# Kernel tuning notes

Hardware: AMD Instinct MI355X
Metric: run time of the kernel (lower is better)

Reference implementation:

```python
import jax, jax.numpy as jnp
import numpy as np
from jax import lax

# Per-tensor power-of-two scales (ScalingImplType.CONST / POWER_OF_TWO in Brevitas)
S_ACT8 = 2.0 ** -4   # 8-bit signed input quant scale
S_ACT4 = 2.0 ** -1   # 4-bit signed input quant scale
S_W = 2.0 ** -2      # per-tensor weight quant scale
S_RELU = 2.0 ** -2   # 4-bit unsigned QuantReLU scale


def fq(x, scale, qmin, qmax):
    # fake-quant with straight-through estimator (STE)
    q = jnp.clip(jnp.round(x / scale), qmin, qmax) * scale
    return x + lax.stop_gradient(q - x)


def fq_signed(x, scale, bits):
    return fq(x, scale, -(2 ** (bits - 1)), 2 ** (bits - 1) - 1)


def fq_uint(x, scale, bits):
    return fq(x, scale, 0, 2 ** bits - 1)


def qconv(x, w, in_bits, w_bits, s_in, stride=1, padding=0, groups=1):
    xq = fq_signed(x, s_in, in_bits)
    wq = fq_signed(w, S_W, w_bits)
    return lax.conv_general_dilated(
        xq, wq, (stride, stride), [(padding, padding)] * 2,
        feature_group_count=groups,
        dimension_numbers=('NCHW', 'OIHW', 'NCHW'))


def maxpool(x, k, s):
    return lax.reduce_window(x, -jnp.inf, lax.max,
                             (1, 1, k, k), (1, 1, s, s), 'VALID')


def dwsep(x, dw, pw):
    c = x.shape[1]
    x = qconv(x, dw, 4, 4, S_ACT4, padding=1, groups=c)  # depthwise 3x3
    x = qconv(x, pw, 4, 4, S_ACT4)                       # pointwise 1x1
    return x


def qrelu4(x):
    return fq_uint(jax.nn.relu(x), S_RELU, 4)


def setup_inputs() -> dict:
    key = jax.random.key(0)
    ks = jax.random.split(key, 10)
    B = 1024
    mk = lambda k, shp, sc=0.5: jax.random.normal(k, shp, jnp.float32) * sc
    return {
        'x': jax.random.normal(ks[0], (B, 3, 32, 32), jnp.float32),
        'w0': mk(ks[1], (3, 3, 1, 1)),
        'dw1': mk(ks[2], (3, 1, 3, 3)),
        'pw1': mk(ks[3], (32, 3, 1, 1)),
        'dw2': mk(ks[4], (32, 1, 3, 3)),
        'pw2': mk(ks[5], (64, 32, 1, 1)),
        'dw3': mk(ks[6], (64, 1, 3, 3)),
        'pw3': mk(ks[7], (128, 64, 1, 1)),
        'wc1': mk(ks[8], (256, 128, 1, 1)),
        'wc2': mk(ks[9], (10, 256, 1, 1)),
    }


def reference(x, w0, dw1, pw1, dw2, pw2, dw3, pw3, wc1, wc2):
    # features
    h = qconv(x, w0, 8, 8, S_ACT8)            # 1x1, 3->3, 8-bit
    h = dwsep(h, dw1, pw1)                    # 3->32, 32x32
    h = qrelu4(h)
    h = maxpool(h, 2, 2)                      # 16x16
    h = dwsep(h, dw2, pw2)                    # 32->64
    h = qrelu4(h)
    h = maxpool(h, 2, 2)                      # 8x8
    h = dwsep(h, dw3, pw3)                    # 64->128
    h = qrelu4(h)
    h = maxpool(h, 8, 1)                      # 1x1
    # classifier
    h = qconv(h, wc1, 4, 4, S_ACT4)           # 128->256
    h = qrelu4(h)
    h = qconv(h, wc2, 4, 4, S_ACT4)           # 256->10
    h = fq_signed(h, S_ACT8, 8)               # output quant int8
    return h
```

## Files before the change

kernel.cpp:

```cpp
#include <hip/hip_runtime.h>

typedef int v4i __attribute__((ext_vector_type(4)));

#define W0i   0
#define DW1i  9
#define PW1i  36
#define DW2i  132
#define DW3i  420
#define PW2p  996
#define PW3p  1508
#define WC1p  3556
#define WC2p  11748
#define PW2Fb 12388
#define PW3Fb 12900
#define WTOT  14948

__device__ __forceinline__ int iclamp(int v, int lo, int hi) {
  return v < lo ? lo : (v > hi ? hi : v);
}
__device__ __forceinline__ int rne4(int a) {
  return (a + 1 + ((a >> 2) & 1)) >> 2;
}
__device__ __forceinline__ int rne32(int a) {
  return (a + 15 + ((a >> 5) & 1)) >> 5;
}

__device__ __forceinline__ int dot4(int a, int b, int c) {
#if defined(__has_builtin) && __has_builtin(__builtin_amdgcn_sdot4)
  return __builtin_amdgcn_sdot4(a, b, c, false);
#else
  c += ((a << 24) >> 24) * ((b << 24) >> 24);
  c += ((a << 16) >> 24) * ((b << 16) >> 24);
  c += ((a <<  8) >> 24) * ((b <<  8) >> 24);
  c += (a >> 24) * (b >> 24);
  return c;
#endif
}

__device__ __forceinline__ int alignb(int hi, int lo, int sh) {
#if defined(__has_builtin) && __has_builtin(__builtin_amdgcn_alignbyte)
  return __builtin_amdgcn_alignbyte(hi, lo, sh);
#else
  return (int)(((((unsigned long long)(unsigned)hi) << 32) |
                (unsigned)lo) >> (8 * sh));
#endif
}

__device__ __forceinline__ int pack3(int a, int b, int c) {
  return (a & 0xff) | ((b & 0xff) << 8) | ((c & 0xff) << 16);
}

__global__ __launch_bounds__(256) void prep_weights(
    const float* __restrict__ w0,  const float* __restrict__ dw1,
    const float* __restrict__ pw1, const float* __restrict__ dw2,
    const float* __restrict__ pw2, const float* __restrict__ dw3,
    const float* __restrict__ pw3, const float* __restrict__ wc1,
    const float* __restrict__ wc2, int* __restrict__ ws) {
  int t = blockIdx.x * blockDim.x + threadIdx.x;
  if (t >= WTOT) return;
  if (t < PW2p) {
    float w; int lo = -8, hi = 7;
    if (t < DW1i)      { w = w0[t];        lo = -128; hi = 127; }
    else if (t < PW1i)   w = dw1[t - DW1i];
    else if (t < DW2i)   w = pw1[t - PW1i];
    else if (t < DW3i)   w = dw2[t - DW2i];
    else                 w = dw3[t - DW3i];
    ws[t] = iclamp((int)rintf(w * 4.f), lo, hi);
  } else if (t < PW2Fb) {
    const float* src;
    if (t < WC1p) {
      if (t < PW3p) src = pw2 + (t - PW2p) * 4;
      else          src = pw3 + (t - PW3p) * 4;
    } else {
      if (t < WC2p) src = wc1 + (t - WC1p) * 4;
      else          src = wc2 + (t - WC2p) * 4;
    }
    int p = 0;
#pragma unroll
    for (int b = 0; b < 4; b++) {
      int c = iclamp((int)rintf(src[b] * 4.f), -8, 7);
      p |= (c & 0xff) << (8 * b);
    }
    ws[t] = p;
  } else if (t < PW3Fb) {
    int i = t - PW2Fb;
    int nt = i >> 7, r = i & 127, lane = r >> 1, dw = r & 1;
    int n = nt * 16 + (lane & 15);
    int kb = (lane >> 4) * 8 + dw * 4;
    int p = 0;
#pragma unroll
    for (int b = 0; b < 4; b++) {
      int c = iclamp((int)rintf(pw2[n * 32 + kb + b] * 4.f), -8, 7);
      p |= (c & 0xff) << (8 * b);
    }
    ws[t] = p;
  } else {
    int i = t - PW3Fb;
    int g = i >> 7, r = i & 127, lane = r >> 1, dw = r & 1;
    int nt = g >> 1, kh = g & 1;
    int n = nt * 16 + (lane & 15);
    int kb = kh * 32 + (lane >> 4) * 8 + dw * 4;
    int p = 0;
#pragma unroll
    for (int b = 0; b < 4; b++) {
      int c = iclamp((int)rintf(pw3[n * 64 + kb + b] * 4.f), -8, 7);
      p |= (c & 0xff) << (8 * b);
    }
    ws[t] = p;
  }
}

__global__ __launch_bounds__(256, 4) void fused_net(
    const float* __restrict__ x,
    const int*   __restrict__ wq,
    float* __restrict__ out)
{
  const int img = blockIdx.x;
  const int tid = threadIdx.x;

  __shared__ __align__(16) int bufAi[2560];
  __shared__ __align__(16) int bufBi[2592];
  __shared__ int s_red[256];

  {
    const float* xim = x + (size_t)img * 3072;
    const int p4 = tid * 4;
    float4 v0 = *(const float4*)(xim + p4);
    float4 v1 = *(const float4*)(xim + 1024 + p4);
    float4 v2 = *(const float4*)(xim + 2048 + p4);
    int w[9];
#pragma unroll
    for (int i = 0; i < 9; i++) w[i] = wq[W0i + i];
#define Q8(v) iclamp((int)rintf((v) * 16.f), -128, 127)
    int a0[4] = {Q8(v0.x), Q8(v0.y), Q8(v0.z), Q8(v0.w)};
    int a1[4] = {Q8(v1.x), Q8(v1.y), Q8(v1.z), Q8(v1.w)};
    int a2[4] = {Q8(v2.x), Q8(v2.y), Q8(v2.z), Q8(v2.w)};
#undef Q8
#pragma unroll
    for (int o = 0; o < 3; o++) {
      int pk = 0;
#pragma unroll
      for (int j = 0; j < 4; j++) {
        int s = a0[j] * w[o * 3] + a1[j] * w[o * 3 + 1] + a2[j] * w[o * 3 + 2];
        pk |= (iclamp(rne32(s), -8, 7) & 0xff) << (8 * j);
      }
      bufAi[o * 256 + tid] = pk;
    }
  }
  __syncthreads();

  {
    const int y = tid >> 3, q = tid & 7;
#pragma unroll
    for (int c = 0; c < 3; c++) {
      int wr[3];
#pragma unroll
      for (int r = 0; r < 3; r++)
        wr[r] = pack3(wq[DW1i + c * 9 + r * 3], wq[DW1i + c * 9 + r * 3 + 1],
                      wq[DW1i + c * 9 + r * 3 + 2]);
      const int* ap = bufAi + c * 256;
      int acc0 = 0, acc1 = 0, acc2 = 0, acc3 = 0;
#pragma unroll
      for (int ky = 0; ky < 3; ky++) {
        int yy = y + ky - 1;
        if (yy < 0 || yy > 31) continue;
        int base = yy * 8 + q;
        int dC = ap[base];
        int dL = q ? ap[base - 1] : 0;
        int dR = (q < 7) ? ap[base + 1] : 0;
        int w = wr[ky];
        acc0 = dot4(alignb(dC, dL, 3), w, acc0);
        acc1 = dot4(dC, w, acc1);
        acc2 = dot4(alignb(dR, dC, 1), w, acc2);
        acc3 = dot4(alignb(dR, dC, 2), w, acc3);
      }
      int pk = (iclamp(rne4(acc0), -8, 7) & 0xff) |
               ((iclamp(rne4(acc1), -8, 7) & 0xff) << 8) |
               ((iclamp(rne4(acc2), -8, 7) & 0xff) << 16) |
               ((iclamp(rne4(acc3), -8, 7) & 0xff) << 24);
      bufBi[c * 256 + tid] = pk;
    }
  }
  __syncthreads();

  {
    const int py = tid >> 4, px = tid & 15;
    const signed char* bB = (const signed char*)bufBi;
    int a[4];
#pragma unroll
    for (int d = 0; d < 4; d++) {
      int sp = (2 * py + (d >> 1)) * 32 + 2 * px + (d & 1);
      a[d] = pack3(bB[sp], bB[1024 + sp], bB[2048 + sp]);
    }
#pragma unroll
    for (int it = 0; it < 8; it++) {
      int pk = 0;
#pragma unroll
      for (int j = 0; j < 4; j++) {
        int o = it * 4 + j;
        int wpk = pack3(wq[PW1i + o * 3], wq[PW1i + o * 3 + 1],
                        wq[PW1i + o * 3 + 2]);
        int m0 = dot4(a[0], wpk, 0), m1 = dot4(a[1], wpk, 0);
        int m2 = dot4(a[2], wpk, 0), m3 = dot4(a[3], wpk, 0);
        int mx = max(max(m0, m1), max(m2, m3));
        pk |= iclamp(rne4(mx), 0, 7) << (8 * j);
      }
      bufAi[py * 149 + px * 9 + it] = pk;
    }
  }
  __syncthreads();

  for (int it2 = 0; it2 < 2; it2++) {
    int idx = tid + 256 * it2;
    int cq = __builtin_amdgcn_readfirstlane(idx >> 6);
    int s = idx & 63;
    int y = s >> 2, x0 = (s & 3) << 2;
    int wk[9][4];
#pragma unroll
    for (int t9 = 0; t9 < 9; t9++)
#pragma unroll
      for (int cc = 0; cc < 4; cc++)
        wk[t9][cc] = wq[DW2i + (cq * 4 + cc) * 9 + t9];
    int acc[4][4] = {};
#pragma unroll
    for (int ky = 0; ky < 3; ky++) {
      int yy = y + ky - 1;
      if (yy < 0 || yy > 15) continue;
      int rb = yy * 149 + cq;
      int rd[6];
      rd[0] = (x0 > 0) ? bufAi[rb + (x0 - 1) * 9] : 0;
      rd[1] = bufAi[rb + x0 * 9];
      rd[2] = bufAi[rb + (x0 + 1) * 9];
      rd[3] = bufAi[rb + (x0 + 2) * 9];
      rd[4] = bufAi[rb + (x0 + 3) * 9];
      rd[5] = (x0 < 12) ? bufAi[rb + (x0 + 4) * 9] : 0;
      int e[6][4];
#pragma unroll
      for (int k = 0; k < 6; k++)
#pragma unroll
        for (int cc = 0; cc < 4; cc++) e[k][cc] = (rd[k] >> (8 * cc)) & 0xf;
#pragma unroll
      for (int j = 0; j < 4; j++)
#pragma unroll
        for (int kx = 0; kx < 3; kx++)
#pragma unroll
          for (int cc = 0; cc < 4; cc++)
            acc[j][cc] += e[j + kx][cc] * wk[ky * 3 + kx][cc];
    }
#pragma unroll
    for (int j = 0; j < 4; j++) {
      int pk = 0;
#pragma unroll
      for (int cc = 0; cc < 4; cc++)
        pk |= (iclamp(rne4(acc[j][cc]), -8, 7) & 0xff) << (8 * cc);
      bufBi[y * 162 + (x0 + j) * 10 + cq] = pk;
    }
  }
  __syncthreads();

#pragma unroll
  for (int i = 0; i < 4; i++) {
    int id = tid + 256 * i;
    int m = id >> 2, c2 = id & 3;
    int qp = m >> 2, d = m & 3;
    int sy = ((qp >> 3) << 1) + (d >> 1);
    int sx = ((qp & 7) << 1) + (d & 1);
    long v = *(const long*)(bufBi + sy * 162 + sx * 10 + c2 * 2);
    *(long*)(bufAi + m * 10 + c2 * 2) = v;
  }
  __syncthreads();

  {
    const int w = tid >> 6, lane = tid & 63;
    const int lm = lane & 15, kg = lane >> 4;
    const long bw = *(const long*)(wq + PW2Fb + (w * 64 + lane) * 2);
    const signed char* Ab = (const signed char*)bufAi;
    signed char* A2c = (signed char*)bufBi;
    const int n = w * 16 + lm;
#pragma unroll 4
    for (int mt = 0; mt < 16; mt++) {
      int m = mt * 16 + lm;
      long av = *(const long*)(Ab + m * 40 + kg * 8);
      v4i d = __builtin_amdgcn_mfma_i32_16x16x32_i8(av, bw, (v4i){0, 0, 0, 0},
                                                    0, 0, 0);
      int mx = max(max(d[0], d[1]), max(d[2], d[3]));
      int qp = mt * 4 + kg;
      int py = qp >> 3, px = qp & 7;
      A2c[(py * 137 + px * 17 + (n >> 2)) * 4 + (n & 3)] =
          (signed char)iclamp(rne4(mx), 0, 7);
    }
  }
  __syncthreads();

  {
    int cq2 = tid >> 4;
    int s = tid & 15;
    int y = s >> 1, x0 = (s & 1) << 2;
    int wk[9][4];
#pragma unroll
    for (int t9 = 0; t9 < 9; t9++)
#pragma unroll
      for (int cc = 0; cc < 4; cc++)
        wk[t9][cc] = wq[DW3i + (cq2 * 4 + cc) * 9 + t9];
    int acc[4][4] = {};
#pragma unroll
    for (int ky = 0; ky < 3; ky++) {
      int yy = y + ky - 1;
      if (yy < 0 || yy > 7) continue;
      int rb = yy * 137 + cq2;
      int rd[6];
      rd[0] = (x0 == 4) ? bufBi[rb + (x0 - 1) * 17] : 0;
      rd[1] = bufBi[rb + x0 * 17];
      rd[2] = bufBi[rb + (x0 + 1) * 17];
      rd[3] = bufBi[rb + (x0 + 2) * 17];
      rd[4] = bufBi[rb + (x0 + 3) * 17];
      rd[5] = (x0 == 0) ? bufBi[rb + (x0 + 4) * 17] : 0;
      int e[6][4];
#pragma unroll
      for (int k = 0; k < 6; k++)
#pragma unroll
        for (int cc = 0; cc < 4; cc++) e[k][cc] = (rd[k] >> (8 * cc)) & 0xf;
#pragma unroll
      for (int j = 0; j < 4; j++)
#pragma unroll
        for (int kx = 0; kx < 3; kx++)
#pragma unroll
          for (int cc = 0; cc < 4; cc++)
            acc[j][cc] += e[j + kx][cc] * wk[ky * 3 + kx][cc];
    }
#pragma unroll
    for (int j = 0; j < 4; j++) {
      int pk = 0;
#pragma unroll
      for (int cc = 0; cc < 4; cc++)
        pk |= (iclamp(rne4(acc[j][cc]), -8, 7) & 0xff) << (8 * cc);
      bufAi[(y * 8 + x0 + j) * 18 + cq2] = pk;
    }
  }
  __syncthreads();

  {
    const int w = tid >> 6, lane = tid & 63;
    const int lm = lane & 15, kg = lane >> 4;
    const signed char* Ab = (const signed char*)bufAi;
    signed char* fcin = (signed char*)bufBi;
#pragma unroll
    for (int h = 0; h < 2; h++) {
      int nt = w * 2 + h;
      const long b0 = *(const long*)(wq + PW3Fb + (nt * 2 + 0) * 128 + lane * 2);
      const long b1 = *(const long*)(wq + PW3Fb + (nt * 2 + 1) * 128 + lane * 2);
      int mx = -1000000;
#pragma unroll
      for (int mt = 0; mt < 4; mt++) {
        int m = mt * 16 + lm;
        long a0 = *(const long*)(Ab + m * 72 + kg * 8);
        long a1 = *(const long*)(Ab + m * 72 + 32 + kg * 8);
        v4i d = __builtin_amdgcn_mfma_i32_16x16x32_i8(a0, b0, (v4i){0, 0, 0, 0},
                                                      0, 0, 0);
        d = __builtin_amdgcn_mfma_i32_16x16x32_i8(a1, b1, d, 0, 0, 0);
        int t4 = max(max(d[0], d[1]), max(d[2], d[3]));
        mx = mx > t4 ? mx : t4;
      }
      mx = max(mx, __shfl_xor(mx, 16));
      mx = max(mx, __shfl_xor(mx, 32));
      if (lane < 16)
        fcin[nt * 16 + lm] = (signed char)iclamp(rne4(mx), 0, 7);
    }
  }
  __syncthreads();

  {
    const int4* wp = (const int4*)(wq + WC1p + tid * 32);
    const int4* mp = (const int4*)bufBi;
    int acc = 0;
#pragma unroll
    for (int rI = 0; rI < 8; rI++) {
      int4 a = mp[rI]; int4 w = wp[rI];
      acc = dot4(a.x, w.x, acc); acc = dot4(a.y, w.y, acc);
      acc = dot4(a.z, w.z, acc); acc = dot4(a.w, w.w, acc);
    }
    ((signed char*)bufAi)[tid] = (signed char)iclamp(rne4(acc), 0, 7);
  }
  __syncthreads();

  if (tid < 80) {
    int k = tid >> 3, j = tid & 7;
    const int4* wp = (const int4*)(wq + WC2p + k * 64 + j * 8);
    int4 w0v = wp[0], w1v = wp[1];
    const int4* ap = (const int4*)bufAi;
    int4 A0 = ap[j * 2], A1 = ap[j * 2 + 1];
    int acc = dot4(A0.x, w0v.x, 0);
    acc = dot4(A0.y, w0v.y, acc); acc = dot4(A0.z, w0v.z, acc);
    acc = dot4(A0.w, w0v.w, acc);
    acc = dot4(A1.x, w1v.x, acc); acc = dot4(A1.y, w1v.y, acc);
    acc = dot4(A1.z, w1v.z, acc); acc = dot4(A1.w, w1v.w, acc);
    s_red[tid] = acc;
  }
  __syncthreads();
  if (tid < 10) {
    int acc = 0;
#pragma unroll
    for (int j = 0; j < 8; j++) acc += s_red[tid * 8 + j];
    int code = iclamp(2 * acc, -128, 127);
    out[(size_t)img * 10 + tid] = (float)code * 0.0625f;
  }
}

extern "C" void kernel_launch(void* const* d_in, const int* in_sizes, int n_in,
                              void* d_out, int out_size, void* d_ws, size_t ws_size,
                              hipStream_t stream) {
  const float* x   = (const float*)d_in[0];
  const float* w0  = (const float*)d_in[1];
  const float* dw1 = (const float*)d_in[2];
  const float* pw1 = (const float*)d_in[3];
  const float* dw2 = (const float*)d_in[4];
  const float* pw2 = (const float*)d_in[5];
  const float* dw3 = (const float*)d_in[6];
  const float* pw3 = (const float*)d_in[7];
  const float* wc1 = (const float*)d_in[8];
  const float* wc2 = (const float*)d_in[9];
  int*   wsq = (int*)d_ws;
  float* out = (float*)d_out;

  prep_weights<<<(WTOT + 255) / 256, 256, 0, stream>>>(
      w0, dw1, pw1, dw2, pw2, dw3, pw3, wc1, wc2, wsq);
  fused_net<<<1024, 256, 0, stream>>>(x, wsq, out);
}
```

Baseline: 97.88 us.

## Use packed int16 SIMD for depthwise convs and reuse A fragments across MFMA tiles

The depthwise 3x3 convs for stages 2 and 3 now split each packed 4-channel word into even and odd 16-bit lanes and accumulate with v_pk_mad_i16. A packed RNE/clamp routine replaces the per-channel scalar multiply-adds and requantization, and a new prep layout stores the depthwise weights as packed 16-bit pairs. Pointwise stage 2 is re-tiled so each wave computes two N-tiles over half the M range, and stage 3 loads each A fragment once for two N-tiles. The stage-1 pointwise input gather uses byte permutes instead of separate byte loads. This cuts VALU instruction count, at the cost of inline asm and reliance on int16 accumulators not overflowing.

```diff
diff --git a/kernel.cpp b/kernel.cpp
--- a/kernel.cpp
+++ b/kernel.cpp
@@ -13,7 +13,9 @@
 #define WC2p  11748
 #define PW2Fb 12388
 #define PW3Fb 12900
-#define WTOT  14948
+#define DW2pk 14948
+#define DW3pk 15092
+#define WTOT  15380
 
 __device__ __forceinline__ int iclamp(int v, int lo, int hi) {
   return v < lo ? lo : (v > hi ? hi : v);
@@ -48,6 +50,49 @@
 
 __device__ __forceinline__ int pack3(int a, int b, int c) {
   return (a & 0xff) | ((b & 0xff) << 8) | ((c & 0xff) << 16);
+}
+
+__device__ __forceinline__ int pk_mad16(int a, int b, int c) {
+  int d;
+  asm("v_pk_mad_i16 %0, %1, %2, %3" : "=v"(d) : "v"(a), "v"(b), "v"(c));
+  return d;
+}
+__device__ __forceinline__ int pk_add16(int a, int b) {
+  int d;
+  asm("v_pk_add_i16 %0, %1, %2" : "=v"(d) : "v"(a), "v"(b));
+  return d;
+}
+__device__ __forceinline__ int pk_ashr16(int sh, int a) {
+  int d;
+  asm("v_pk_ashrrev_i16 %0, %1, %2" : "=v"(d) : "v"(sh), "v"(a));
+  return d;
+}
+__device__ __forceinline__ int pk_max16(int a, int b) {
+  int d;
+  asm("v_pk_max_i16 %0, %1, %2" : "=v"(d) : "v"(a), "v"(b));
+  return d;
+}
+__device__ __forceinline__ int pk_min16(int a, int b) {
+  int d;
+  asm("v_pk_min_i16 %0, %1, %2" : "=v"(d) : "v"(a), "v"(b));
+  return d;
+}
+__device__ __forceinline__ int rne4s_pk(int a) {
+  const int sh = 0x00020002, one = 0x00010001;
+  int t = pk_ashr16(sh, a);
+  t &= one;
+  t += one;
+  int s4 = pk_add16(a, t);
+  int r = pk_ashr16(sh, s4);
+  r = pk_max16(r, (int)0xFFF8FFF8);
+  r = pk_min16(r, 0x00070007);
+  return r;
+}
+
+__device__ __forceinline__ int max4(v4i d) {
+  int a = d[0] > d[1] ? d[0] : d[1];
+  int b = d[2] > d[3] ? d[2] : d[3];
+  return a > b ? a : b;
 }
 
 __global__ __launch_bounds__(256) void prep_weights(
@@ -94,7 +139,7 @@
       p |= (c & 0xff) << (8 * b);
     }
     ws[t] = p;
-  } else {
+  } else if (t < DW2pk) {
     int i = t - PW3Fb;
     int g = i >> 7, r = i & 127, lane = r >> 1, dw = r & 1;
     int nt = g >> 1, kh = g & 1;
@@ -107,6 +152,18 @@
       p |= (c & 0xff) << (8 * b);
     }
     ws[t] = p;
+  } else if (t < DW3pk) {
+    int i = t - DW2pk;
+    int cq = i / 18, r = i - cq * 18, t9 = r >> 1, par = r & 1;
+    int wl = iclamp((int)rintf(dw2[(cq * 4 + par) * 9 + t9] * 4.f), -8, 7);
+    int wh = iclamp((int)rintf(dw2[(cq * 4 + 2 + par) * 9 + t9] * 4.f), -8, 7);
+    ws[t] = (wl & 0xFFFF) | (wh << 16);
+  } else {
+    int i = t - DW3pk;
+    int cq = i / 18, r = i - cq * 18, t9 = r >> 1, par = r & 1;
+    int wl = iclamp((int)rintf(dw3[(cq * 4 + par) * 9 + t9] * 4.f), -8, 7);
+    int wh = iclamp((int)rintf(dw3[(cq * 4 + 2 + par) * 9 + t9] * 4.f), -8, 7);
+    ws[t] = (wl & 0xFFFF) | (wh << 16);
   }
 }
 
@@ -185,12 +242,22 @@
 
   {
     const int py = tid >> 4, px = tid & 15;
-    const signed char* bB = (const signed char*)bufBi;
+    const unsigned char* bB = (const unsigned char*)bufBi;
+    unsigned u[3][2];
+#pragma unroll
+    for (int c = 0; c < 3; c++)
+#pragma unroll
+      for (int dy = 0; dy < 2; dy++)
+        u[c][dy] = *(const unsigned short*)(bB + c * 1024 +
+                                            (2 * py + dy) * 32 + 2 * px);
     int a[4];
 #pragma unroll
     for (int d = 0; d < 4; d++) {
-      int sp = (2 * py + (d >> 1)) * 32 + 2 * px + (d & 1);
-      a[d] = pack3(bB[sp], bB[1024 + sp], bB[2048 + sp]);
+      int dy = d >> 1, dx = d & 1;
+      unsigned t1 = __builtin_amdgcn_perm(u[1][dy], u[0][dy],
+                                          0x0C0C0000u | ((4 + dx) << 8) | dx);
+      a[d] = (int)__builtin_amdgcn_perm(u[2][dy], t1,
+                                        0x0C000100u | ((4 + dx) << 16));
     }
 #pragma unroll
     for (int it = 0; it < 8; it++) {
@@ -215,13 +282,13 @@
     int cq = __builtin_amdgcn_readfirstlane(idx >> 6);
     int s = idx & 63;
     int y = s >> 2, x0 = (s & 3) << 2;
-    int wk[9][4];
-#pragma unroll
-    for (int t9 = 0; t9 < 9; t9++)
-#pragma unroll
-      for (int cc = 0; cc < 4; cc++)
-        wk[t9][cc] = wq[DW2i + (cq * 4 + cc) * 9 + t9];
-    int acc[4][4] = {};
+    int we[9], wo[9];
+    {
+      const int2* wp = (const int2*)(wq + DW2pk + cq * 18);
+#pragma unroll
+      for (int t9 = 0; t9 < 9; t9++) { int2 v = wp[t9]; we[t9] = v.x; wo[t9] = v.y; }
+    }
+    int acce[4] = {}, acco[4] = {};
 #pragma unroll
     for (int ky = 0; ky < 3; ky++) {
       int yy = y + ky - 1;
@@ -234,26 +301,26 @@
       rd[3] = bufAi[rb + (x0 + 2) * 9];
       rd[4] = bufAi[rb + (x0 + 3) * 9];
       rd[5] = (x0 < 12) ? bufAi[rb + (x0 + 4) * 9] : 0;
-      int e[6][4];
-#pragma unroll
-      for (int k = 0; k < 6; k++)
-#pragma unroll
-        for (int cc = 0; cc < 4; cc++) e[k][cc] = (rd[k] >> (8 * cc)) & 0xf;
+      int ee[6], eo[6];
+#pragma unroll
+      for (int k = 0; k < 6; k++) {
+        ee[k] = rd[k] & 0x000F000F;
+        eo[k] = (rd[k] >> 8) & 0x000F000F;
+      }
 #pragma unroll
       for (int j = 0; j < 4; j++)
 #pragma unroll
-        for (int kx = 0; kx < 3; kx++)
-#pragma unroll
-          for (int cc = 0; cc < 4; cc++)
-            acc[j][cc] += e[j + kx][cc] * wk[ky * 3 + kx][cc];
+        for (int kx = 0; kx < 3; kx++) {
+          acce[j] = pk_mad16(ee[j + kx], we[ky * 3 + kx], acce[j]);
+          acco[j] = pk_mad16(eo[j + kx], wo[ky * 3 + kx], acco[j]);
+        }
     }
 #pragma unroll
     for (int j = 0; j < 4; j++) {
-      int pk = 0;
-#pragma unroll
-      for (int cc = 0; cc < 4; cc++)
-        pk |= (iclamp(rne4(acc[j][cc]), -8, 7) & 0xff) << (8 * cc);
-      bufBi[y * 162 + (x0 + j) * 10 + cq] = pk;
+      int re = rne4s_pk(acce[j]);
+      int ro = rne4s_pk(acco[j]);
+      bufBi[y * 162 + (x0 + j) * 10 + cq] =
+          (re & 0x00FF00FF) | ((ro & 0x00FF00FF) << 8);
     }
   }
   __syncthreads();
@@ -273,21 +340,26 @@
   {
     const int w = tid >> 6, lane = tid & 63;
     const int lm = lane & 15, kg = lane >> 4;
-    const long bw = *(const long*)(wq + PW2Fb + (w * 64 + lane) * 2);
+    const int ntp = (w & 1) * 2;
+    const int mtb = (w >> 1) * 8;
+    const long bw0 = *(const long*)(wq + PW2Fb + (ntp * 64 + lane) * 2);
+    const long bw1 = *(const long*)(wq + PW2Fb + ((ntp + 1) * 64 + lane) * 2);
     const signed char* Ab = (const signed char*)bufAi;
     signed char* A2c = (signed char*)bufBi;
-    const int n = w * 16 + lm;
+    const int n0 = ntp * 16 + lm, n1 = (ntp + 1) * 16 + lm;
 #pragma unroll 4
-    for (int mt = 0; mt < 16; mt++) {
+    for (int mt = mtb; mt < mtb + 8; mt++) {
       int m = mt * 16 + lm;
       long av = *(const long*)(Ab + m * 40 + kg * 8);
-      v4i d = __builtin_amdgcn_mfma_i32_16x16x32_i8(av, bw, (v4i){0, 0, 0, 0},
-                                                    0, 0, 0);
-      int mx = max(max(d[0], d[1]), max(d[2], d[3]));
+      v4i d0 = __builtin_amdgcn_mfma_i32_16x16x32_i8(av, bw0, (v4i){0, 0, 0, 0},
+                                                     0, 0, 0);
+      v4i d1 = __builtin_amdgcn_mfma_i32_16x16x32_i8(av, bw1, (v4i){0, 0, 0, 0},
+                                                     0, 0, 0);
       int qp = mt * 4 + kg;
       int py = qp >> 3, px = qp & 7;
-      A2c[(py * 137 + px * 17 + (n >> 2)) * 4 + (n & 3)] =
-          (signed char)iclamp(rne4(mx), 0, 7);
+      int bb = (py * 137 + px * 17) * 4;
+      A2c[bb + n0] = (signed char)iclamp(rne4(max4(d0)), 0, 7);
+      A2c[bb + n1] = (signed char)iclamp(rne4(max4(d1)), 0, 7);
     }
   }
   __syncthreads();
@@ -296,13 +368,13 @@
     int cq2 = tid >> 4;
     int s = tid & 15;
     int y = s >> 1, x0 = (s & 1) << 2;
-    int wk[9][4];
-#pragma unroll
-    for (int t9 = 0; t9 < 9; t9++)
-#pragma unroll
-      for (int cc = 0; cc < 4; cc++)
-        wk[t9][cc] = wq[DW3i + (cq2 * 4 + cc) * 9 + t9];
-    int acc[4][4] = {};
+    int we[9], wo[9];
+    {
+      const int2* wp = (const int2*)(wq + DW3pk + cq2 * 18);
+#pragma unroll
+      for (int t9 = 0; t9 < 9; t9++) { int2 v = wp[t9]; we[t9] = v.x; wo[t9] = v.y; }
+    }
+    int acce[4] = {}, acco[4] = {};
 #pragma unroll
     for (int ky = 0; ky < 3; ky++) {
       int yy = y + ky - 1;
@@ -315,26 +387,26 @@
       rd[3] = bufBi[rb + (x0 + 2) * 17];
       rd[4] = bufBi[rb + (x0 + 3) * 17];
       rd[5] = (x0 == 0) ? bufBi[rb + (x0 + 4) * 17] : 0;
-      int e[6][4];
-#pragma unroll
-      for (int k = 0; k < 6; k++)
-#pragma unroll
-        for (int cc = 0; cc < 4; cc++) e[k][cc] = (rd[k] >> (8 * cc)) & 0xf;
+      int ee[6], eo[6];
+#pragma unroll
+      for (int k = 0; k < 6; k++) {
+        ee[k] = rd[k] & 0x000F000F;
+        eo[k] = (rd[k] >> 8) & 0x000F000F;
+      }
 #pragma unroll
       for (int j = 0; j < 4; j++)
 #pragma unroll
-        for (int kx = 0; kx < 3; kx++)
-#pragma unroll
-          for (int cc = 0; cc < 4; cc++)
-            acc[j][cc] += e[j + kx][cc] * wk[ky * 3 + kx][cc];
+        for (int kx = 0; kx < 3; kx++) {
+          acce[j] = pk_mad16(ee[j + kx], we[ky * 3 + kx], acce[j]);
+          acco[j] = pk_mad16(eo[j + kx], wo[ky * 3 + kx], acco[j]);
+        }
     }
 #pragma unroll
     for (int j = 0; j < 4; j++) {
-      int pk = 0;
-#pragma unroll
-      for (int cc = 0; cc < 4; cc++)
-        pk |= (iclamp(rne4(acc[j][cc]), -8, 7) & 0xff) << (8 * cc);
-      bufAi[(y * 8 + x0 + j) * 18 + cq2] = pk;
+      int re = rne4s_pk(acce[j]);
+      int ro = rne4s_pk(acco[j]);
+      bufAi[(y * 8 + x0 + j) * 18 + cq2] =
+          (re & 0x00FF00FF) | ((ro & 0x00FF00FF) << 8);
     }
   }
   __syncthreads();
@@ -344,27 +416,34 @@
     const int lm = lane & 15, kg = lane >> 4;
     const signed char* Ab = (const signed char*)bufAi;
     signed char* fcin = (signed char*)bufBi;
+    long b0v[2], b1v[2];
 #pragma unroll
     for (int h = 0; h < 2; h++) {
       int nt = w * 2 + h;
-      const long b0 = *(const long*)(wq + PW3Fb + (nt * 2 + 0) * 128 + lane * 2);
-      const long b1 = *(const long*)(wq + PW3Fb + (nt * 2 + 1) * 128 + lane * 2);
-      int mx = -1000000;
-#pragma unroll
-      for (int mt = 0; mt < 4; mt++) {
-        int m = mt * 16 + lm;
-        long a0 = *(const long*)(Ab + m * 72 + kg * 8);
-        long a1 = *(const long*)(Ab + m * 72 + 32 + kg * 8);
-        v4i d = __builtin_amdgcn_mfma_i32_16x16x32_i8(a0, b0, (v4i){0, 0, 0, 0},
-                                                      0, 0, 0);
-        d = __builtin_amdgcn_mfma_i32_16x16x32_i8(a1, b1, d, 0, 0, 0);
-        int t4 = max(max(d[0], d[1]), max(d[2], d[3]));
-        mx = mx > t4 ? mx : t4;
+      b0v[h] = *(const long*)(wq + PW3Fb + (nt * 2 + 0) * 128 + lane * 2);
+      b1v[h] = *(const long*)(wq + PW3Fb + (nt * 2 + 1) * 128 + lane * 2);
+    }
+    int mx[2] = {-1000000, -1000000};
+#pragma unroll
+    for (int mt = 0; mt < 4; mt++) {
+      int m = mt * 16 + lm;
+      long a0 = *(const long*)(Ab + m * 72 + kg * 8);
+      long a1 = *(const long*)(Ab + m * 72 + 32 + kg * 8);
+#pragma unroll
+      for (int h = 0; h < 2; h++) {
+        v4i d = __builtin_amdgcn_mfma_i32_16x16x32_i8(a0, b0v[h],
+                                                      (v4i){0, 0, 0, 0}, 0, 0, 0);
+        d = __builtin_amdgcn_mfma_i32_16x16x32_i8(a1, b1v[h], d, 0, 0, 0);
+        int t4 = max4(d);
+        mx[h] = mx[h] > t4 ? mx[h] : t4;
       }
-      mx = max(mx, __shfl_xor(mx, 16));
-      mx = max(mx, __shfl_xor(mx, 32));
+    }
+#pragma unroll
+    for (int h = 0; h < 2; h++) {
+      int red = max(mx[h], __shfl_xor(mx[h], 16));
+      red = max(red, __shfl_xor(red, 32));
       if (lane < 16)
-        fcin[nt * 16 + lm] = (signed char)iclamp(rne4(mx), 0, 7);
+        fcin[(w * 2 + h) * 16 + lm] = (signed char)iclamp(rne4(red), 0, 7);
     }
   }
   __syncthreads();
```

Result: no change. 95.97 us (-2.0%).
